# Kernel optimization log

Measured on AMD Instinct MI355X. Metric: run time of the kernel, lower is better.

The kernel has to match this reference:

```python
import math
import jax, jax.numpy as jnp
import numpy as np

K_EACH = 64
EPS = 1e-5
EPS_VAR = 1e-4
_GELU_C = math.sqrt(2.0 / math.pi)


def _gelu(x):
    return 0.5 * x * (1.0 + jnp.tanh(_GELU_C * (x + 0.044715 * x * x * x)))


def _topk_mask(score, k):
    # score: [B,T,D] -> bool mask [B,T,D] with True at the top-k per row
    B, T, D = score.shape
    idx = jax.lax.top_k(score, k)[1].reshape(B * T, k)
    rows = jnp.arange(B * T)[:, None]
    m = jnp.zeros((B * T, D), dtype=bool).at[rows, idx].set(True)
    return m.reshape(B, T, D)


def setup_inputs() -> dict:
    key = jax.random.key(0)
    ks = jax.random.split(key, 6)
    B, T, D = 4, 4096, 2048
    x = jax.random.normal(ks[0], (B, T, D), dtype=jnp.float32)
    ema_mean = 0.1 * jax.random.normal(ks[1], (D,), dtype=jnp.float32)
    ema_sq = ema_mean ** 2 + jax.random.uniform(ks[2], (D,), dtype=jnp.float32, minval=0.5, maxval=1.5)
    ema_out_mean = 0.1 * jax.random.normal(ks[3], (D,), dtype=jnp.float32)
    ema_out_sq = ema_out_mean ** 2 + jax.random.uniform(ks[4], (D,), dtype=jnp.float32, minval=0.5, maxval=1.5)
    d_raw = jax.random.normal(ks[5], (D,), dtype=jnp.float32)
    ema_out_dir = d_raw / jnp.linalg.norm(d_raw)
    return {
        "x": x,
        "logit_decay": jnp.asarray(math.log(0.9 / 0.1), jnp.float32),
        "log_tau": jnp.asarray(math.log(2.0), jnp.float32),
        "log_beta": jnp.asarray(math.log(math.exp(0.5) - 1.0), jnp.float32),
        "log_gamma": jnp.asarray(math.log(math.exp(1.0) - 1.0), jnp.float32),
        "ema_mean": ema_mean,
        "ema_sq": ema_sq,
        "ema_out_mean": ema_out_mean,
        "ema_out_sq": ema_out_sq,
        "ema_out_dir": ema_out_dir,
    }


def reference(x, logit_decay, log_tau, log_beta, log_gamma,
              ema_mean, ema_sq, ema_out_mean, ema_out_sq, ema_out_dir):
    # Steady-state (_ready=True) forward of GELU205. logit_decay only affects
    # the EMA state update (a no-grad side effect), not the returned output.
    sg = jax.lax.stop_gradient
    D = x.shape[-1]
    k = min(K_EACH, D)

    tau = jnp.exp(log_tau)
    beta = jax.nn.softplus(log_beta)
    gamma = jax.nn.softplus(log_gamma)

    out = _gelu(x)

    # per-channel z-scores against running stats (no-grad in original)
    var_in = jnp.maximum(ema_sq - ema_mean ** 2, EPS_VAR)
    z_in = sg((sg(x) - ema_mean) / (jnp.sqrt(var_in) + EPS))
    var_out = jnp.maximum(ema_out_sq - ema_out_mean ** 2, EPS_VAR)
    z_out = sg((sg(out) - ema_out_mean) / (jnp.sqrt(var_out) + EPS))

    # dual top-k intersection mask
    mask_in = _topk_mask(jnp.abs(z_in), k)
    mask_out = _topk_mask(jnp.abs(z_out), k)
    inter = mask_in & mask_out

    # channel gate (grads flow to beta, gamma; z_in is detached)
    inter_g = jnp.clip(1.0 + beta * jnp.tanh(gamma * z_in), 0.1, 8.0)
    gate_vec = jnp.where(inter, inter_g, 1.0)

    # cosine-similarity gate (fully no-grad in original, incl. tau)
    out_n = out / jnp.maximum(jnp.linalg.norm(out, axis=-1, keepdims=True), 1e-12)
    ema_n = ema_out_dir / jnp.maximum(jnp.linalg.norm(ema_out_dir), 1e-12)
    cos_sim = jnp.clip(jnp.sum(out_n * ema_n, axis=-1), -1.0, 1.0)
    gate_cos = sg(jnp.exp(-tau * cos_sim))[..., None]

    return out * gate_vec * gate_cos
```

## Files before the change

### kernel.cpp

```cpp
#include <hip/hip_runtime.h>
#include <math.h>
#include <stdint.h>

#define D_    2048
#define BLK   256
#define KSEL  64
#define NBIN  512
#define B0    96
#define CAP   128

typedef float v2f __attribute__((ext_vector_type(2)));

__device__ __forceinline__ float tanh_xla(float x) {
    const float kMax = 7.90531110763549805f;
    float xc = fminf(fmaxf(x, -kMax), kMax);
    float x2 = __fmul_rn(xc, xc);
    float p = -2.76076847742355e-16f;
    p = __fadd_rn(__fmul_rn(p, x2), 2.00018790482477e-13f);
    p = __fadd_rn(__fmul_rn(p, x2), -8.60467152213735e-11f);
    p = __fadd_rn(__fmul_rn(p, x2), 5.12229709037114e-08f);
    p = __fadd_rn(__fmul_rn(p, x2), 1.48572235717979e-05f);
    p = __fadd_rn(__fmul_rn(p, x2), 6.37261928875436e-04f);
    p = __fadd_rn(__fmul_rn(p, x2), 4.89352455891786e-03f);
    float num = __fmul_rn(xc, p);
    float q = 1.19825839466702e-06f;
    q = __fadd_rn(__fmul_rn(q, x2), 1.18534705686654e-04f);
    q = __fadd_rn(__fmul_rn(q, x2), 2.26843463243900e-03f);
    q = __fadd_rn(__fmul_rn(q, x2), 4.89352518554385e-03f);
    float r = __fdiv_rn(num, q);
    return (fabsf(x) < 0.0004f) ? x : r;
}

__device__ __forceinline__ float gelu_exact(float xx) {
    float a = __fmul_rn(0.044715f, xx);
    a = __fmul_rn(a, xx);
    a = __fmul_rn(a, xx);
    float inner = __fadd_rn(xx, a);
    float tg = tanh_xla(__fmul_rn(0.7978845608028654f, inner));
    return __fmul_rn(__fmul_rn(0.5f, xx), __fadd_rn(1.0f, tg));
}

__device__ __forceinline__ float tanh_fast(float y) {
    float e = __builtin_amdgcn_exp2f(y * 2.8853900817779268f);
    return 1.0f - 2.0f * __builtin_amdgcn_rcpf(1.0f + e);
}

__global__ __launch_bounds__(BLK) void prep_kernel(
    const float* __restrict__ m_in, const float* __restrict__ q_in,
    const float* __restrict__ m_out, const float* __restrict__ q_out,
    const float* __restrict__ dirv,
    const float* __restrict__ p_log_tau,
    const float* __restrict__ p_log_beta,
    const float* __restrict__ p_log_gamma,
    float* __restrict__ wsp)
{
    __shared__ float spart[4];
    const int t = threadIdx.x;
    const int c = blockIdx.x * BLK + t;
    if (c < D_) {
        float mi = m_in[c];
        float vi = fmaxf(__fsub_rn(q_in[c], __fmul_rn(mi, mi)), 1e-4f);
        float di = __fadd_rn(__fsqrt_rn(vi), 1e-5f);
        wsp[c]        = di;
        wsp[D_ + c]   = __fdiv_rn(1.0f, di);
        float mo = m_out[c];
        float vo = fmaxf(__fsub_rn(q_out[c], __fmul_rn(mo, mo)), 1e-4f);
        float dd = __fadd_rn(__fsqrt_rn(vo), 1e-5f);
        wsp[2 * D_ + c] = dd;
        wsp[3 * D_ + c] = __fdiv_rn(1.0f, dd);
    }
    if (blockIdx.x == 0) {
        float acc = 0.f;
        #pragma unroll
        for (int k = 0; k < D_ / BLK; ++k) {
            float v = dirv[t + k * BLK];
            acc = fmaf(v, v, acc);
        }
        #pragma unroll
        for (int off = 32; off > 0; off >>= 1) acc += __shfl_xor(acc, off);
        if ((t & 63) == 0) spart[t >> 6] = acc;
        __syncthreads();
        if (t == 0) {
            wsp[4 * D_ + 0] = spart[0] + spart[1] + spart[2] + spart[3];
            wsp[4 * D_ + 1] = expf(p_log_tau[0]);
            wsp[4 * D_ + 2] = log1pf(expf(p_log_beta[0]));
            wsp[4 * D_ + 3] = log1pf(expf(p_log_gamma[0]));
        }
    }
}

__device__ __forceinline__ void scan_find(
    const uint32_t* hist, int wid, int lane,
    int* sBi, int* sGi, int* sBo, int* sGo)
{
    if (wid < 2) {
        const uint32_t* hp = hist + wid * NBIN;
        uint32_t h[8];
        *(uint4*)&h[0] = *(const uint4*)&hp[lane * 8 + 0];
        *(uint4*)&h[4] = *(const uint4*)&hp[lane * 8 + 4];
        uint32_t tot = 0;
        #pragma unroll
        for (int k = 0; k < 8; ++k) tot += h[k];
        uint32_t S = tot;
        #pragma unroll
        for (int d2 = 1; d2 < 64; d2 <<= 1) {
            uint32_t o = __shfl_down(S, d2, 64);
            S += (lane + d2 < 64) ? o : 0u;
        }
        uint32_t run = S - tot;
        #pragma unroll
        for (int k = 7; k >= 0; --k) {
            uint32_t prev = run;
            run += h[k];
            if (run >= (uint32_t)KSEL && prev < (uint32_t)KSEL) {
                if (wid == 0) { *sBi = lane * 8 + k; *sGi = (int)prev; }
                else          { *sBo = lane * 8 + k; *sGo = (int)prev; }
            }
        }
    }
}

__global__ __launch_bounds__(BLK) void gelu205_kernel(
    const float* __restrict__ x,
    const float* __restrict__ ema_mean,
    const float* __restrict__ ema_out_mean,
    const float* __restrict__ ema_out_dir,
    const float* __restrict__ wsp,
    float* __restrict__ out)
{
    __shared__ uint32_t hist[2 * NBIN];
    __shared__ uint32_t cbI[CAP], ciI[CAP], cfI[CAP];
    __shared__ uint32_t cbO[CAP], ciO[CAP], cfO[CAP];
    __shared__ float sred[8];
    __shared__ float sgcos;
    __shared__ int sBi, sGi, sNCi, sBo, sGo, sNCo;

    const int t = threadIdx.x;
    const int row = blockIdx.x;
    const float* xr = x + (size_t)row * D_;
    float* outr = out + (size_t)row * D_;

    const float* den_in  = wsp;
    const float* inv_in  = wsp + D_;
    const float* den_out = wsp + 2 * D_;
    const float* inv_out = wsp + 3 * D_;
    const float dd_row = wsp[4 * D_ + 0];
    const float tau    = wsp[4 * D_ + 1];
    const float beta   = wsp[4 * D_ + 2];
    const float gamma  = wsp[4 * D_ + 3];

    float ov[8], zif[8];
    int bin_in[8], bin_out[8];
    v2f acc_oo = {0.f, 0.f}, acc_od = {0.f, 0.f};

    #pragma unroll
    for (int g = 0; g < 2; ++g) {
        const int base = (g << 10) + t * 4;
        float4 x4  = *(const float4*)(xr + base);
        float4 m4  = *(const float4*)(ema_mean + base);
        float4 i4  = *(const float4*)(inv_in + base);
        float4 mo4 = *(const float4*)(ema_out_mean + base);
        float4 io4 = *(const float4*)(inv_out + base);
        float4 d4  = *(const float4*)(ema_out_dir + base);
        const v2f* xp2  = (const v2f*)&x4;
        const v2f* mp2  = (const v2f*)&m4;
        const v2f* ip2  = (const v2f*)&i4;
        const v2f* mop2 = (const v2f*)&mo4;
        const v2f* iop2 = (const v2f*)&io4;
        const v2f* dp2  = (const v2f*)&d4;
        #pragma unroll
        for (int p = 0; p < 2; ++p) {
            const int j = g * 4 + p * 2;
            v2f xx = xp2[p];
            v2f x2 = xx * xx;
            v2f ax = xx * 0.044715f;
            v2f inner = __builtin_elementwise_fma(ax, x2, xx);
            v2f ea = inner * -2.3022269136469443f;
            v2f ev; ev.x = __builtin_amdgcn_exp2f(ea.x);
            ev.y = __builtin_amdgcn_exp2f(ea.y);
            v2f dn = ev + 1.0f;
            v2f sgm; sgm.x = __builtin_amdgcn_rcpf(dn.x);
            sgm.y = __builtin_amdgcn_rcpf(dn.y);
            v2f o2 = xx * sgm;
            ov[j] = o2.x; ov[j + 1] = o2.y;
            v2f zi2 = (xx - mp2[p]) * ip2[p];
            zif[j] = zi2.x; zif[j + 1] = zi2.y;
            bin_in[j]     = (int)fminf(fabsf(zi2.x) * 64.0f, 511.0f);
            bin_in[j + 1] = (int)fminf(fabsf(zi2.y) * 64.0f, 511.0f);
            v2f zo2 = (o2 - mop2[p]) * iop2[p];
            bin_out[j]     = (int)fminf(fabsf(zo2.x) * 64.0f, 511.0f);
            bin_out[j + 1] = (int)fminf(fabsf(zo2.y) * 64.0f, 511.0f);
            acc_oo = __builtin_elementwise_fma(o2, o2, acc_oo);
            acc_od = __builtin_elementwise_fma(o2, dp2[p], acc_od);
        }
    }
    float s_oo = acc_oo.x + acc_oo.y;
    float s_od = acc_od.x + acc_od.y;

    #pragma unroll
    for (int off = 32; off > 0; off >>= 1) {
        s_oo += __shfl_xor(s_oo, off);
        s_od += __shfl_xor(s_od, off);
    }
    const int wid = t >> 6, lane = t & 63;
    if (lane == 0) {
        sred[wid * 2 + 0] = s_oo;
        sred[wid * 2 + 1] = s_od;
    }

    *(uint4*)&hist[t * 4] = make_uint4(0u, 0u, 0u, 0u);
    if (t == 0) { sNCi = 0; sNCo = 0; sBi = -1; sBo = -1; }
    __syncthreads();

    #pragma unroll
    for (int j = 0; j < 8; ++j) {
        if (bin_in[j] >= B0)  atomicAdd(&hist[bin_in[j]], 1u);
        if (bin_out[j] >= B0) atomicAdd(&hist[NBIN + bin_out[j]], 1u);
    }
    if (t == 0) {
        float oo = sred[0] + sred[2] + sred[4] + sred[6];
        float od = sred[1] + sred[3] + sred[5] + sred[7];
        float no = fmaxf(sqrtf(oo), 1e-12f);
        float nd = fmaxf(sqrtf(dd_row), 1e-12f);
        float cs = fminf(fmaxf(od / (no * nd), -1.0f), 1.0f);
        sgcos = expf(-tau * cs);
    }
    __syncthreads();

    scan_find(hist, wid, lane, &sBi, &sGi, &sBo, &sGo);
    __syncthreads();

    int Bi = sBi, Bo = sBo;
    if (Bi < 0 || Bo < 0) {
        #pragma unroll
        for (int j = 0; j < 8; ++j) {
            if (bin_in[j] < B0)  atomicAdd(&hist[bin_in[j]], 1u);
            if (bin_out[j] < B0) atomicAdd(&hist[NBIN + bin_out[j]], 1u);
        }
        __syncthreads();
        scan_find(hist, wid, lane, &sBi, &sGi, &sBo, &sGo);
        __syncthreads();
        Bi = sBi; Bo = sBo;
    }

    int slotI[8], slotO[8];
    #pragma unroll
    for (int j = 0; j < 8; ++j) {
        slotI[j] = -1;
        slotO[j] = -1;
        const int ch = ((j >> 2) << 10) + t * 4 + (j & 3);
        if (bin_in[j] == Bi) {
            float xx = xr[ch];
            float ze = fabsf(__fdiv_rn(__fsub_rn(xx, ema_mean[ch]), den_in[ch]));
            int sl = atomicAdd(&sNCi, 1);
            if (sl < CAP) {
                cbI[sl] = __float_as_uint(ze);
                ciI[sl] = (uint32_t)ch;
                slotI[j] = sl;
            }
        }
        if (bin_out[j] == Bo) {
            float xx = xr[ch];
            float oe = gelu_exact(xx);
            float ze = fabsf(__fdiv_rn(__fsub_rn(oe, ema_out_mean[ch]), den_out[ch]));
            int sl = atomicAdd(&sNCo, 1);
            if (sl < CAP) {
                cbO[sl] = __float_as_uint(ze);
                ciO[sl] = (uint32_t)ch;
                slotO[j] = sl;
            }
        }
    }
    __syncthreads();

    {
        const int nci = min(sNCi, CAP), nco = min(sNCo, CAP);
        const uint32_t needI = (uint32_t)(KSEL - sGi);
        const uint32_t needO = (uint32_t)(KSEL - sGo);
        if (t < 128) {
            for (int i = t; i < nci; i += 128) {
                uint32_t ui = cbI[i], di = ciI[i], r = 0;
                for (int jj = 0; jj < nci; ++jj) {
                    uint32_t uj = cbI[jj];
                    r += (uj > ui || (uj == ui && ciI[jj] < di)) ? 1u : 0u;
                }
                cfI[i] = (r < needI) ? 1u : 0u;
            }
        } else {
            for (int i = t - 128; i < nco; i += 128) {
                uint32_t ui = cbO[i], di = ciO[i], r = 0;
                for (int jj = 0; jj < nco; ++jj) {
                    uint32_t uj = cbO[jj];
                    r += (uj > ui || (uj == ui && ciO[jj] < di)) ? 1u : 0u;
                }
                cfO[i] = (r < needO) ? 1u : 0u;
            }
        }
    }
    __syncthreads();

    const float gcos = sgcos;
    #pragma unroll
    for (int g = 0; g < 2; ++g) {
        float4 r4;
        float* rp = (float*)&r4;
        #pragma unroll
        for (int l = 0; l < 4; ++l) {
            const int j = g * 4 + l;
            bool selI = (bin_in[j] > Bi) || (slotI[j] >= 0 && cfI[slotI[j]] != 0u);
            bool selO = (bin_out[j] > Bo) || (slotO[j] >= 0 && cfO[slotO[j]] != 0u);
            float gate = 1.0f;
            if (selI && selO) {
                float th = tanh_fast(gamma * zif[j]);
                gate = fminf(fmaxf(fmaf(beta, th, 1.0f), 0.1f), 8.0f);
            }
            rp[l] = ov[j] * gate * gcos;
        }
        *(float4*)(outr + (g << 10) + t * 4) = r4;
    }
}

extern "C" void kernel_launch(void* const* d_in, const int* in_sizes, int n_in,
                              void* d_out, int out_size, void* d_ws, size_t ws_size,
                              hipStream_t stream) {
    const float* x            = (const float*)d_in[0];
    const float* p_log_tau    = (const float*)d_in[2];
    const float* p_log_beta   = (const float*)d_in[3];
    const float* p_log_gamma  = (const float*)d_in[4];
    const float* ema_mean     = (const float*)d_in[5];
    const float* ema_sq       = (const float*)d_in[6];
    const float* ema_out_mean = (const float*)d_in[7];
    const float* ema_out_sq   = (const float*)d_in[8];
    const float* ema_out_dir  = (const float*)d_in[9];
    float* wsp = (float*)d_ws;
    const int rows = in_sizes[0] / D_;

    prep_kernel<<<(D_ + BLK - 1) / BLK, BLK, 0, stream>>>(
        ema_mean, ema_sq, ema_out_mean, ema_out_sq, ema_out_dir,
        p_log_tau, p_log_beta, p_log_gamma, wsp);
    gelu205_kernel<<<rows, BLK, 0, stream>>>(
        x, ema_mean, ema_out_mean, ema_out_dir, wsp,
        (float*)d_out);
}
```

Baseline: 75.03 us.

## Process two rows per block with packed bins and per-wave scans

Each block now handles two rows, which halves the grid and shares the per-channel stat loads between the rows. Each of the four wavefronts scans one of the four histograms. The in and out bin indices are packed into one register, and per-element zif and slot arrays are replaced by a linear search of candidate channel lists plus recomputing z_in from global memory. The aim is to amortize setup and sync overhead and lower register pressure, at the cost of halving the block count to 8192 and adding a per-element candidate search.

New measurement: 122.4 us. 1.63x slower.

```diff
diff --git a/kernel.cpp b/kernel.cpp
--- a/kernel.cpp
+++ b/kernel.cpp
@@ -43,6 +43,32 @@
 __device__ __forceinline__ float tanh_fast(float y) {
     float e = __builtin_amdgcn_exp2f(y * 2.8853900817779268f);
     return 1.0f - 2.0f * __builtin_amdgcn_rcpf(1.0f + e);
+}
+
+__device__ __forceinline__ void elem2(
+    v2f xx, v2f m, v2f iv, v2f mo, v2f io, v2f dv,
+    float* ovp, uint32_t* bpp, v2f* aoo, v2f* aod)
+{
+    v2f x2 = xx * xx;
+    v2f ax = xx * 0.044715f;
+    v2f inner = __builtin_elementwise_fma(ax, x2, xx);
+    v2f ea = inner * -2.3022269136469443f;
+    v2f ev; ev.x = __builtin_amdgcn_exp2f(ea.x);
+    ev.y = __builtin_amdgcn_exp2f(ea.y);
+    v2f dn = ev + 1.0f;
+    v2f sg; sg.x = __builtin_amdgcn_rcpf(dn.x);
+    sg.y = __builtin_amdgcn_rcpf(dn.y);
+    v2f o2 = xx * sg;
+    ovp[0] = o2.x; ovp[1] = o2.y;
+    v2f zi = (xx - m) * iv;
+    v2f zo = (o2 - mo) * io;
+    v2f c511 = {511.0f, 511.0f};
+    v2f bi = __builtin_elementwise_min(__builtin_elementwise_abs(zi) * 64.0f, c511);
+    v2f bo = __builtin_elementwise_min(__builtin_elementwise_abs(zo) * 64.0f, c511);
+    bpp[0] = (uint32_t)(int)bi.x | ((uint32_t)(int)bo.x << 16);
+    bpp[1] = (uint32_t)(int)bi.y | ((uint32_t)(int)bo.y << 16);
+    *aoo = __builtin_elementwise_fma(o2, o2, *aoo);
+    *aod = __builtin_elementwise_fma(o2, dv, *aod);
 }
 
 __global__ __launch_bounds__(BLK) void prep_kernel(
@@ -89,35 +115,42 @@
     }
 }
 
-__device__ __forceinline__ void scan_find(
-    const uint32_t* hist, int wid, int lane,
-    int* sBi, int* sGi, int* sBo, int* sGo)
+__device__ __forceinline__ void scan_one(
+    const uint32_t* hp, volatile uint32_t* scr2, int lane)
 {
-    if (wid < 2) {
-        const uint32_t* hp = hist + wid * NBIN;
-        uint32_t h[8];
-        *(uint4*)&h[0] = *(const uint4*)&hp[lane * 8 + 0];
-        *(uint4*)&h[4] = *(const uint4*)&hp[lane * 8 + 4];
-        uint32_t tot = 0;
-        #pragma unroll
-        for (int k = 0; k < 8; ++k) tot += h[k];
-        uint32_t S = tot;
-        #pragma unroll
-        for (int d2 = 1; d2 < 64; d2 <<= 1) {
-            uint32_t o = __shfl_down(S, d2, 64);
-            S += (lane + d2 < 64) ? o : 0u;
-        }
-        uint32_t run = S - tot;
-        #pragma unroll
-        for (int k = 7; k >= 0; --k) {
-            uint32_t prev = run;
-            run += h[k];
-            if (run >= (uint32_t)KSEL && prev < (uint32_t)KSEL) {
-                if (wid == 0) { *sBi = lane * 8 + k; *sGi = (int)prev; }
-                else          { *sBo = lane * 8 + k; *sGo = (int)prev; }
-            }
-        }
-    }
+    uint32_t h[8];
+    *(uint4*)&h[0] = *(const uint4*)&hp[lane * 8 + 0];
+    *(uint4*)&h[4] = *(const uint4*)&hp[lane * 8 + 4];
+    uint32_t tot = 0;
+    #pragma unroll
+    for (int k = 0; k < 8; ++k) tot += h[k];
+    uint32_t S = tot;
+    #pragma unroll
+    for (int d = 1; d < 64; d <<= 1) {
+        uint32_t o = __shfl_down(S, d, 64);
+        S += (lane + d < 64) ? o : 0u;
+    }
+    uint32_t run = S - tot;
+    #pragma unroll
+    for (int k = 7; k >= 0; --k) {
+        uint32_t prev = run;
+        run += h[k];
+        if (run >= (uint32_t)KSEL && prev < (uint32_t)KSEL) {
+            scr2[0] = (uint32_t)(lane * 8 + k);
+            scr2[1] = prev;
+        }
+    }
+}
+
+__device__ __forceinline__ bool sel_one(
+    uint32_t bin, int B, const uint32_t* ci, const uint32_t* cf,
+    int nc, uint32_t ch)
+{
+    if ((int)bin > B) return true;
+    if ((int)bin != B) return false;
+    for (int jj = 0; jj < nc; ++jj)
+        if (ci[jj] == ch) return cf[jj] != 0u;
+    return false;
 }
 
 __global__ __launch_bounds__(BLK) void gelu205_kernel(
@@ -126,19 +159,22 @@
     const float* __restrict__ ema_out_mean,
     const float* __restrict__ ema_out_dir,
     const float* __restrict__ wsp,
-    float* __restrict__ out)
+    float* __restrict__ out,
+    int nrows)
 {
-    __shared__ uint32_t hist[2 * NBIN];
-    __shared__ uint32_t cbI[CAP], ciI[CAP], cfI[CAP];
-    __shared__ uint32_t cbO[CAP], ciO[CAP], cfO[CAP];
-    __shared__ float sred[8];
-    __shared__ float sgcos;
-    __shared__ int sBi, sGi, sNCi, sBo, sGo, sNCo;
+    __shared__ uint32_t lds[2048 + 4 * 3 * CAP + 16];
+    uint32_t* hist = lds;
+    uint32_t* scr  = lds + 2048 + 4 * 3 * CAP;
 
     const int t = threadIdx.x;
-    const int row = blockIdx.x;
-    const float* xr = x + (size_t)row * D_;
-    float* outr = out + (size_t)row * D_;
+    const int lane = t & 63, wid = t >> 6;
+    const int r0 = blockIdx.x * 2, r1 = r0 + 1;
+    const bool has2 = (r1 < nrows);
+
+    const float* xr0 = x + (size_t)r0 * D_;
+    const float* xr1 = x + (size_t)r1 * D_;
+    float* outr0 = out + (size_t)r0 * D_;
+    float* outr1 = out + (size_t)r1 * D_;
 
     const float* den_in  = wsp;
     const float* inv_in  = wsp + D_;
@@ -149,174 +185,228 @@
     const float beta   = wsp[4 * D_ + 2];
     const float gamma  = wsp[4 * D_ + 3];
 
-    float ov[8], zif[8];
-    int bin_in[8], bin_out[8];
-    v2f acc_oo = {0.f, 0.f}, acc_od = {0.f, 0.f};
+    {
+        uint4 z4 = make_uint4(0u, 0u, 0u, 0u);
+        *(uint4*)&hist[t * 8 + 0] = z4;
+        *(uint4*)&hist[t * 8 + 4] = z4;
+    }
+    if (t < 12) scr[t] = (t < 8 && (t & 1) == 0) ? 0xffffffffu : 0u;
+
+    float ov0[8], ov1[8];
+    uint32_t bp0[8], bp1[8];
+    v2f aoo0 = {0.f, 0.f}, aod0 = {0.f, 0.f};
+    v2f aoo1 = {0.f, 0.f}, aod1 = {0.f, 0.f};
 
     #pragma unroll
     for (int g = 0; g < 2; ++g) {
-        const int base = (g << 10) + t * 4;
-        float4 x4  = *(const float4*)(xr + base);
+        const int base = (g << 10) + (t << 2);
         float4 m4  = *(const float4*)(ema_mean + base);
         float4 i4  = *(const float4*)(inv_in + base);
         float4 mo4 = *(const float4*)(ema_out_mean + base);
         float4 io4 = *(const float4*)(inv_out + base);
         float4 d4  = *(const float4*)(ema_out_dir + base);
-        const v2f* xp2  = (const v2f*)&x4;
+        float4 xa  = *(const float4*)(xr0 + base);
+        float4 xb;
+        if (has2) xb = *(const float4*)(xr1 + base);
+        else xb = make_float4(0.f, 0.f, 0.f, 0.f);
         const v2f* mp2  = (const v2f*)&m4;
         const v2f* ip2  = (const v2f*)&i4;
         const v2f* mop2 = (const v2f*)&mo4;
         const v2f* iop2 = (const v2f*)&io4;
         const v2f* dp2  = (const v2f*)&d4;
+        const v2f* xa2  = (const v2f*)&xa;
+        const v2f* xb2  = (const v2f*)&xb;
         #pragma unroll
         for (int p = 0; p < 2; ++p) {
             const int j = g * 4 + p * 2;
-            v2f xx = xp2[p];
-            v2f x2 = xx * xx;
-            v2f ax = xx * 0.044715f;
-            v2f inner = __builtin_elementwise_fma(ax, x2, xx);
-            v2f ea = inner * -2.3022269136469443f;
-            v2f ev; ev.x = __builtin_amdgcn_exp2f(ea.x);
-            ev.y = __builtin_amdgcn_exp2f(ea.y);
-            v2f dn = ev + 1.0f;
-            v2f sgm; sgm.x = __builtin_amdgcn_rcpf(dn.x);
-            sgm.y = __builtin_amdgcn_rcpf(dn.y);
-            v2f o2 = xx * sgm;
-            ov[j] = o2.x; ov[j + 1] = o2.y;
-            v2f zi2 = (xx - mp2[p]) * ip2[p];
-            zif[j] = zi2.x; zif[j + 1] = zi2.y;
-            bin_in[j]     = (int)fminf(fabsf(zi2.x) * 64.0f, 511.0f);
-            bin_in[j + 1] = (int)fminf(fabsf(zi2.y) * 64.0f, 511.0f);
-            v2f zo2 = (o2 - mop2[p]) * iop2[p];
-            bin_out[j]     = (int)fminf(fabsf(zo2.x) * 64.0f, 511.0f);
-            bin_out[j + 1] = (int)fminf(fabsf(zo2.y) * 64.0f, 511.0f);
-            acc_oo = __builtin_elementwise_fma(o2, o2, acc_oo);
-            acc_od = __builtin_elementwise_fma(o2, dp2[p], acc_od);
-        }
-    }
-    float s_oo = acc_oo.x + acc_oo.y;
-    float s_od = acc_od.x + acc_od.y;
-
+            elem2(xa2[p], mp2[p], ip2[p], mop2[p], iop2[p], dp2[p],
+                  &ov0[j], &bp0[j], &aoo0, &aod0);
+            elem2(xb2[p], mp2[p], ip2[p], mop2[p], iop2[p], dp2[p],
+                  &ov1[j], &bp1[j], &aoo1, &aod1);
+        }
+    }
+
+    float oo0 = aoo0.x + aoo0.y, od0 = aod0.x + aod0.y;
+    float oo1 = aoo1.x + aoo1.y, od1 = aod1.x + aod1.y;
     #pragma unroll
     for (int off = 32; off > 0; off >>= 1) {
-        s_oo += __shfl_xor(s_oo, off);
-        s_od += __shfl_xor(s_od, off);
-    }
-    const int wid = t >> 6, lane = t & 63;
+        oo0 += __shfl_xor(oo0, off);
+        od0 += __shfl_xor(od0, off);
+        oo1 += __shfl_xor(oo1, off);
+        od1 += __shfl_xor(od1, off);
+    }
+    __shared__ float sred[16];
     if (lane == 0) {
-        sred[wid * 2 + 0] = s_oo;
-        sred[wid * 2 + 1] = s_od;
-    }
-
-    *(uint4*)&hist[t * 4] = make_uint4(0u, 0u, 0u, 0u);
-    if (t == 0) { sNCi = 0; sNCo = 0; sBi = -1; sBo = -1; }
+        sred[wid * 4 + 0] = oo0;
+        sred[wid * 4 + 1] = od0;
+        sred[wid * 4 + 2] = oo1;
+        sred[wid * 4 + 3] = od1;
+    }
     __syncthreads();
 
+    float gcos0, gcos1;
+    {
+        float foo0 = sred[0] + sred[4] + sred[8] + sred[12];
+        float fod0 = sred[1] + sred[5] + sred[9] + sred[13];
+        float foo1 = sred[2] + sred[6] + sred[10] + sred[14];
+        float fod1 = sred[3] + sred[7] + sred[11] + sred[15];
+        float nd = fmaxf(sqrtf(dd_row), 1e-12f);
+        float no0 = fmaxf(sqrtf(foo0), 1e-12f);
+        float cs0 = fminf(fmaxf(fod0 / (no0 * nd), -1.0f), 1.0f);
+        gcos0 = expf(-tau * cs0);
+        float no1 = fmaxf(sqrtf(foo1), 1e-12f);
+        float cs1 = fminf(fmaxf(fod1 / (no1 * nd), -1.0f), 1.0f);
+        gcos1 = expf(-tau * cs1);
+    }
+
     #pragma unroll
     for (int j = 0; j < 8; ++j) {
-        if (bin_in[j] >= B0)  atomicAdd(&hist[bin_in[j]], 1u);
-        if (bin_out[j] >= B0) atomicAdd(&hist[NBIN + bin_out[j]], 1u);
-    }
-    if (t == 0) {
-        float oo = sred[0] + sred[2] + sred[4] + sred[6];
-        float od = sred[1] + sred[3] + sred[5] + sred[7];
-        float no = fmaxf(sqrtf(oo), 1e-12f);
-        float nd = fmaxf(sqrtf(dd_row), 1e-12f);
-        float cs = fminf(fmaxf(od / (no * nd), -1.0f), 1.0f);
-        sgcos = expf(-tau * cs);
+        uint32_t bi = bp0[j] & 0xffffu, bo = bp0[j] >> 16;
+        if (bi >= (uint32_t)B0) atomicAdd(&hist[bi], 1u);
+        if (bo >= (uint32_t)B0) atomicAdd(&hist[NBIN + bo], 1u);
+    }
+    if (has2) {
+        #pragma unroll
+        for (int j = 0; j < 8; ++j) {
+            uint32_t bi = bp1[j] & 0xffffu, bo = bp1[j] >> 16;
+            if (bi >= (uint32_t)B0) atomicAdd(&hist[2 * NBIN + bi], 1u);
+            if (bo >= (uint32_t)B0) atomicAdd(&hist[3 * NBIN + bo], 1u);
+        }
     }
     __syncthreads();
 
-    scan_find(hist, wid, lane, &sBi, &sGi, &sBo, &sGo);
+    scan_one(hist + wid * NBIN, scr + 2 * wid, lane);
     __syncthreads();
 
-    int Bi = sBi, Bo = sBo;
-    if (Bi < 0 || Bo < 0) {
+    int BI0 = (int)scr[0], BO0 = (int)scr[2];
+    int BI1 = (int)scr[4], BO1 = (int)scr[6];
+
+    bool fb = (BI0 < 0) | (BO0 < 0) | (has2 & ((BI1 < 0) | (BO1 < 0)));
+    if (fb) {
         #pragma unroll
         for (int j = 0; j < 8; ++j) {
-            if (bin_in[j] < B0)  atomicAdd(&hist[bin_in[j]], 1u);
-            if (bin_out[j] < B0) atomicAdd(&hist[NBIN + bin_out[j]], 1u);
+            uint32_t bi = bp0[j] & 0xffffu, bo = bp0[j] >> 16;
+            if (BI0 < 0 && bi < (uint32_t)B0) atomicAdd(&hist[bi], 1u);
+            if (BO0 < 0 && bo < (uint32_t)B0) atomicAdd(&hist[NBIN + bo], 1u);
+        }
+        if (has2) {
+            #pragma unroll
+            for (int j = 0; j < 8; ++j) {
+                uint32_t bi = bp1[j] & 0xffffu, bo = bp1[j] >> 16;
+                if (BI1 < 0 && bi < (uint32_t)B0) atomicAdd(&hist[2 * NBIN + bi], 1u);
+                if (BO1 < 0 && bo < (uint32_t)B0) atomicAdd(&hist[3 * NBIN + bo], 1u);
+            }
         }
         __syncthreads();
-        scan_find(hist, wid, lane, &sBi, &sGi, &sBo, &sGo);
+        scan_one(hist + wid * NBIN, scr + 2 * wid, lane);
         __syncthreads();
-        Bi = sBi; Bo = sBo;
-    }
-
-    int slotI[8], slotO[8];
+        BI0 = (int)scr[0]; BO0 = (int)scr[2];
+        BI1 = (int)scr[4]; BO1 = (int)scr[6];
+    }
+
+    uint32_t* cb0 = lds + 2048;
+    uint32_t* cb1 = cb0 + 3 * CAP;
+    uint32_t* cb2 = cb1 + 3 * CAP;
+    uint32_t* cb3 = cb2 + 3 * CAP;
+
     #pragma unroll
     for (int j = 0; j < 8; ++j) {
-        slotI[j] = -1;
-        slotO[j] = -1;
-        const int ch = ((j >> 2) << 10) + t * 4 + (j & 3);
-        if (bin_in[j] == Bi) {
-            float xx = xr[ch];
+        const int ch = ((j >> 2) << 10) + (t << 2) + (j & 3);
+        if ((int)(bp0[j] & 0xffffu) == BI0) {
+            float xx = xr0[ch];
             float ze = fabsf(__fdiv_rn(__fsub_rn(xx, ema_mean[ch]), den_in[ch]));
-            int sl = atomicAdd(&sNCi, 1);
-            if (sl < CAP) {
-                cbI[sl] = __float_as_uint(ze);
-                ciI[sl] = (uint32_t)ch;
-                slotI[j] = sl;
-            }
-        }
-        if (bin_out[j] == Bo) {
-            float xx = xr[ch];
+            uint32_t sl = atomicAdd(&scr[8], 1u);
+            if (sl < CAP) { cb0[sl] = __float_as_uint(ze); cb0[CAP + sl] = (uint32_t)ch; }
+        }
+        if ((int)(bp0[j] >> 16) == BO0) {
+            float xx = xr0[ch];
             float oe = gelu_exact(xx);
             float ze = fabsf(__fdiv_rn(__fsub_rn(oe, ema_out_mean[ch]), den_out[ch]));
-            int sl = atomicAdd(&sNCo, 1);
-            if (sl < CAP) {
-                cbO[sl] = __float_as_uint(ze);
-                ciO[sl] = (uint32_t)ch;
-                slotO[j] = sl;
+            uint32_t sl = atomicAdd(&scr[9], 1u);
+            if (sl < CAP) { cb1[sl] = __float_as_uint(ze); cb1[CAP + sl] = (uint32_t)ch; }
+        }
+        if (has2) {
+            if ((int)(bp1[j] & 0xffffu) == BI1) {
+                float xx = xr1[ch];
+                float ze = fabsf(__fdiv_rn(__fsub_rn(xx, ema_mean[ch]), den_in[ch]));
+                uint32_t sl = atomicAdd(&scr[10], 1u);
+                if (sl < CAP) { cb2[sl] = __float_as_uint(ze); cb2[CAP + sl] = (uint32_t)ch; }
+            }
+            if ((int)(bp1[j] >> 16) == BO1) {
+                float xx = xr1[ch];
+                float oe = gelu_exact(xx);
+                float ze = fabsf(__fdiv_rn(__fsub_rn(oe, ema_out_mean[ch]), den_out[ch]));
+                uint32_t sl = atomicAdd(&scr[11], 1u);
+                if (sl < CAP) { cb3[sl] = __float_as_uint(ze); cb3[CAP + sl] = (uint32_t)ch; }
             }
         }
     }
     __syncthreads();
 
     {
-        const int nci = min(sNCi, CAP), nco = min(sNCo, CAP);
-        const uint32_t needI = (uint32_t)(KSEL - sGi);
-        const uint32_t needO = (uint32_t)(KSEL - sGo);
-        if (t < 128) {
-            for (int i = t; i < nci; i += 128) {
-                uint32_t ui = cbI[i], di = ciI[i], r = 0;
-                for (int jj = 0; jj < nci; ++jj) {
-                    uint32_t uj = cbI[jj];
-                    r += (uj > ui || (uj == ui && ciI[jj] < di)) ? 1u : 0u;
+        uint32_t* cbw = lds + 2048 + wid * 3 * CAP;
+        int Bw = (int)scr[2 * wid];
+        if (Bw >= 0) {
+            const int nc = min((int)scr[8 + wid], CAP);
+            const uint32_t need = (uint32_t)(KSEL - (int)scr[2 * wid + 1]);
+            for (int i = lane; i < nc; i += 64) {
+                uint32_t ui = cbw[i], di = cbw[CAP + i], r = 0;
+                for (int jj = 0; jj < nc; ++jj) {
+                    uint32_t uj = cbw[jj];
+                    r += (uj > ui || (uj == ui && cbw[CAP + jj] < di)) ? 1u : 0u;
                 }
-                cfI[i] = (r < needI) ? 1u : 0u;
-            }
-        } else {
-            for (int i = t - 128; i < nco; i += 128) {
-                uint32_t ui = cbO[i], di = ciO[i], r = 0;
-                for (int jj = 0; jj < nco; ++jj) {
-                    uint32_t uj = cbO[jj];
-                    r += (uj > ui || (uj == ui && ciO[jj] < di)) ? 1u : 0u;
-                }
-                cfO[i] = (r < needO) ? 1u : 0u;
+                cbw[2 * CAP + i] = (r < need) ? 1u : 0u;
             }
         }
     }
     __syncthreads();
 
-    const float gcos = sgcos;
-    #pragma unroll
-    for (int g = 0; g < 2; ++g) {
+    const int nc0 = min((int)scr[8], CAP),  nc1 = min((int)scr[9], CAP);
+    const int nc2 = min((int)scr[10], CAP), nc3 = min((int)scr[11], CAP);
+
+    #pragma unroll
+    for (int k = 0; k < 2; ++k) {
         float4 r4;
         float* rp = (float*)&r4;
         #pragma unroll
         for (int l = 0; l < 4; ++l) {
-            const int j = g * 4 + l;
-            bool selI = (bin_in[j] > Bi) || (slotI[j] >= 0 && cfI[slotI[j]] != 0u);
-            bool selO = (bin_out[j] > Bo) || (slotO[j] >= 0 && cfO[slotO[j]] != 0u);
+            const int j = k * 4 + l;
+            const uint32_t ch = (uint32_t)(((j >> 2) << 10) + (t << 2) + (j & 3));
+            bool selI = sel_one(bp0[j] & 0xffffu, BI0, cb0 + CAP, cb0 + 2 * CAP, nc0, ch);
+            bool selO = sel_one(bp0[j] >> 16,     BO0, cb1 + CAP, cb1 + 2 * CAP, nc1, ch);
             float gate = 1.0f;
             if (selI && selO) {
-                float th = tanh_fast(gamma * zif[j]);
+                float xx = xr0[ch];
+                float zi = (xx - ema_mean[ch]) * inv_in[ch];
+                float th = tanh_fast(gamma * zi);
                 gate = fminf(fmaxf(fmaf(beta, th, 1.0f), 0.1f), 8.0f);
             }
-            rp[l] = ov[j] * gate * gcos;
-        }
-        *(float4*)(outr + (g << 10) + t * 4) = r4;
+            rp[l] = ov0[j] * gate * gcos0;
+        }
+        *(float4*)(outr0 + (k << 10) + (t << 2)) = r4;
+    }
+    if (has2) {
+        #pragma unroll
+        for (int k = 0; k < 2; ++k) {
+            float4 r4;
+            float* rp = (float*)&r4;
+            #pragma unroll
+            for (int l = 0; l < 4; ++l) {
+                const int j = k * 4 + l;
+                const uint32_t ch = (uint32_t)(((j >> 2) << 10) + (t << 2) + (j & 3));
+                bool selI = sel_one(bp1[j] & 0xffffu, BI1, cb2 + CAP, cb2 + 2 * CAP, nc2, ch);
+                bool selO = sel_one(bp1[j] >> 16,     BO1, cb3 + CAP, cb3 + 2 * CAP, nc3, ch);
+                float gate = 1.0f;
+                if (selI && selO) {
+                    float xx = xr1[ch];
+                    float zi = (xx - ema_mean[ch]) * inv_in[ch];
+                    float th = tanh_fast(gamma * zi);
+                    gate = fminf(fmaxf(fmaf(beta, th, 1.0f), 0.1f), 8.0f);
+                }
+                rp[l] = ov1[j] * gate * gcos1;
+            }
+            *(float4*)(outr1 + (k << 10) + (t << 2)) = r4;
+        }
     }
 }
 
@@ -338,7 +428,7 @@
     prep_kernel<<<(D_ + BLK - 1) / BLK, BLK, 0, stream>>>(
         ema_mean, ema_sq, ema_out_mean, ema_out_sq, ema_out_dir,
         p_log_tau, p_log_beta, p_log_gamma, wsp);
-    gelu205_kernel<<<rows, BLK, 0, stream>>>(
+    gelu205_kernel<<<(rows + 1) / 2, BLK, 0, stream>>>(
         x, ema_mean, ema_out_mean, ema_out_dir, wsp,
-        (float*)d_out);
-}
+        (float*)d_out, rows);
+}
```

## Process multiple rows per block with prefetch of next row's input

Applied to the files above, without the earlier changes.

Each block now handles 8 rows in a loop instead of one, and prefetches the next row's x values into registers while the current row's histogram and selection phases run. This aims to hide global load latency behind the synchronization-heavy top-k phases and to amortize block launch overhead. In exchange the grid shrinks from 16384 to 2048 blocks, which could reduce latency hiding from concurrent blocks and leave tail imbalance across CUs.

After: 176.1 us. +134.7%, slower.

```diff
diff --git a/kernel.cpp b/kernel.cpp
--- a/kernel.cpp
+++ b/kernel.cpp
@@ -8,6 +8,7 @@
 #define NBIN  512
 #define B0    96
 #define CAP   128
+#define RPB   8
 
 typedef float v2f __attribute__((ext_vector_type(2)));
 
@@ -126,7 +127,8 @@
     const float* __restrict__ ema_out_mean,
     const float* __restrict__ ema_out_dir,
     const float* __restrict__ wsp,
-    float* __restrict__ out)
+    float* __restrict__ out,
+    int nrows)
 {
     __shared__ uint32_t hist[2 * NBIN];
     __shared__ uint32_t cbI[CAP], ciI[CAP], cfI[CAP];
@@ -136,187 +138,207 @@
     __shared__ int sBi, sGi, sNCi, sBo, sGo, sNCo;
 
     const int t = threadIdx.x;
-    const int row = blockIdx.x;
-    const float* xr = x + (size_t)row * D_;
-    float* outr = out + (size_t)row * D_;
-
-    const float* den_in  = wsp;
-    const float* inv_in  = wsp + D_;
-    const float* den_out = wsp + 2 * D_;
-    const float* inv_out = wsp + 3 * D_;
-    const float dd_row = wsp[4 * D_ + 0];
-    const float tau    = wsp[4 * D_ + 1];
-    const float beta   = wsp[4 * D_ + 2];
-    const float gamma  = wsp[4 * D_ + 3];
-
-    float ov[8], zif[8];
-    int bin_in[8], bin_out[8];
-    v2f acc_oo = {0.f, 0.f}, acc_od = {0.f, 0.f};
-
-    #pragma unroll
-    for (int g = 0; g < 2; ++g) {
-        const int base = (g << 10) + t * 4;
-        float4 x4  = *(const float4*)(xr + base);
-        float4 m4  = *(const float4*)(ema_mean + base);
-        float4 i4  = *(const float4*)(inv_in + base);
-        float4 mo4 = *(const float4*)(ema_out_mean + base);
-        float4 io4 = *(const float4*)(inv_out + base);
-        float4 d4  = *(const float4*)(ema_out_dir + base);
-        const v2f* xp2  = (const v2f*)&x4;
-        const v2f* mp2  = (const v2f*)&m4;
-        const v2f* ip2  = (const v2f*)&i4;
-        const v2f* mop2 = (const v2f*)&mo4;
-        const v2f* iop2 = (const v2f*)&io4;
-        const v2f* dp2  = (const v2f*)&d4;
-        #pragma unroll
-        for (int p = 0; p < 2; ++p) {
-            const int j = g * 4 + p * 2;
-            v2f xx = xp2[p];
-            v2f x2 = xx * xx;
-            v2f ax = xx * 0.044715f;
-            v2f inner = __builtin_elementwise_fma(ax, x2, xx);
-            v2f ea = inner * -2.3022269136469443f;
-            v2f ev; ev.x = __builtin_amdgcn_exp2f(ea.x);
-            ev.y = __builtin_amdgcn_exp2f(ea.y);
-            v2f dn = ev + 1.0f;
-            v2f sgm; sgm.x = __builtin_amdgcn_rcpf(dn.x);
-            sgm.y = __builtin_amdgcn_rcpf(dn.y);
-            v2f o2 = xx * sgm;
-            ov[j] = o2.x; ov[j + 1] = o2.y;
-            v2f zi2 = (xx - mp2[p]) * ip2[p];
-            zif[j] = zi2.x; zif[j + 1] = zi2.y;
-            bin_in[j]     = (int)fminf(fabsf(zi2.x) * 64.0f, 511.0f);
-            bin_in[j + 1] = (int)fminf(fabsf(zi2.y) * 64.0f, 511.0f);
-            v2f zo2 = (o2 - mop2[p]) * iop2[p];
-            bin_out[j]     = (int)fminf(fabsf(zo2.x) * 64.0f, 511.0f);
-            bin_out[j + 1] = (int)fminf(fabsf(zo2.y) * 64.0f, 511.0f);
-            acc_oo = __builtin_elementwise_fma(o2, o2, acc_oo);
-            acc_od = __builtin_elementwise_fma(o2, dp2[p], acc_od);
-        }
-    }
-    float s_oo = acc_oo.x + acc_oo.y;
-    float s_od = acc_od.x + acc_od.y;
-
-    #pragma unroll
-    for (int off = 32; off > 0; off >>= 1) {
-        s_oo += __shfl_xor(s_oo, off);
-        s_od += __shfl_xor(s_od, off);
-    }
-    const int wid = t >> 6, lane = t & 63;
-    if (lane == 0) {
-        sred[wid * 2 + 0] = s_oo;
-        sred[wid * 2 + 1] = s_od;
-    }
-
-    *(uint4*)&hist[t * 4] = make_uint4(0u, 0u, 0u, 0u);
-    if (t == 0) { sNCi = 0; sNCo = 0; sBi = -1; sBo = -1; }
-    __syncthreads();
-
-    #pragma unroll
-    for (int j = 0; j < 8; ++j) {
-        if (bin_in[j] >= B0)  atomicAdd(&hist[bin_in[j]], 1u);
-        if (bin_out[j] >= B0) atomicAdd(&hist[NBIN + bin_out[j]], 1u);
-    }
-    if (t == 0) {
-        float oo = sred[0] + sred[2] + sred[4] + sred[6];
-        float od = sred[1] + sred[3] + sred[5] + sred[7];
-        float no = fmaxf(sqrtf(oo), 1e-12f);
-        float nd = fmaxf(sqrtf(dd_row), 1e-12f);
-        float cs = fminf(fmaxf(od / (no * nd), -1.0f), 1.0f);
-        sgcos = expf(-tau * cs);
-    }
-    __syncthreads();
-
-    scan_find(hist, wid, lane, &sBi, &sGi, &sBo, &sGo);
-    __syncthreads();
-
-    int Bi = sBi, Bo = sBo;
-    if (Bi < 0 || Bo < 0) {
+    const int lane = t & 63, wid = t >> 6;
+    const int row0 = blockIdx.x * RPB;
+    if (row0 >= nrows) return;
+
+    float4 xn0, xn1;
+    {
+        const float* xr = x + (size_t)row0 * D_;
+        xn0 = *(const float4*)(xr + (t << 2));
+        xn1 = *(const float4*)(xr + 1024 + (t << 2));
+    }
+
+    for (int k = 0; k < RPB; ++k) {
+        const int row = row0 + k;
+        if (row >= nrows) break;
+        const float* xr = x + (size_t)row * D_;
+        float* outr = out + (size_t)row * D_;
+
+        asm volatile("" ::: "memory");
+
+        const float dd_row = wsp[4 * D_ + 0];
+        const float tau    = wsp[4 * D_ + 1];
+        const float beta   = wsp[4 * D_ + 2];
+        const float gamma  = wsp[4 * D_ + 3];
+
+        float4 xcur[2];
+        xcur[0] = xn0;
+        xcur[1] = xn1;
+
+        float ov[8], zif[8];
+        int bin_in[8], bin_out[8];
+        v2f acc_oo = {0.f, 0.f}, acc_od = {0.f, 0.f};
+
+        #pragma unroll
+        for (int g = 0; g < 2; ++g) {
+            const int base = (g << 10) + (t << 2);
+            float4 m4  = *(const float4*)(ema_mean + base);
+            float4 i4  = *(const float4*)(wsp + D_ + base);
+            float4 mo4 = *(const float4*)(ema_out_mean + base);
+            float4 io4 = *(const float4*)(wsp + 3 * D_ + base);
+            float4 d4  = *(const float4*)(ema_out_dir + base);
+            const v2f* xp2  = (const v2f*)&xcur[g];
+            const v2f* mp2  = (const v2f*)&m4;
+            const v2f* ip2  = (const v2f*)&i4;
+            const v2f* mop2 = (const v2f*)&mo4;
+            const v2f* iop2 = (const v2f*)&io4;
+            const v2f* dp2  = (const v2f*)&d4;
+            #pragma unroll
+            for (int p = 0; p < 2; ++p) {
+                const int j = g * 4 + p * 2;
+                v2f xx = xp2[p];
+                v2f x2 = xx * xx;
+                v2f ax = xx * 0.044715f;
+                v2f inner = __builtin_elementwise_fma(ax, x2, xx);
+                v2f ea = inner * -2.3022269136469443f;
+                v2f ev; ev.x = __builtin_amdgcn_exp2f(ea.x);
+                ev.y = __builtin_amdgcn_exp2f(ea.y);
+                v2f dn = ev + 1.0f;
+                v2f sgm; sgm.x = __builtin_amdgcn_rcpf(dn.x);
+                sgm.y = __builtin_amdgcn_rcpf(dn.y);
+                v2f o2 = xx * sgm;
+                ov[j] = o2.x; ov[j + 1] = o2.y;
+                v2f zi2 = (xx - mp2[p]) * ip2[p];
+                zif[j] = zi2.x; zif[j + 1] = zi2.y;
+                bin_in[j]     = (int)fminf(fabsf(zi2.x) * 64.0f, 511.0f);
+                bin_in[j + 1] = (int)fminf(fabsf(zi2.y) * 64.0f, 511.0f);
+                v2f zo2 = (o2 - mop2[p]) * iop2[p];
+                bin_out[j]     = (int)fminf(fabsf(zo2.x) * 64.0f, 511.0f);
+                bin_out[j + 1] = (int)fminf(fabsf(zo2.y) * 64.0f, 511.0f);
+                acc_oo = __builtin_elementwise_fma(o2, o2, acc_oo);
+                acc_od = __builtin_elementwise_fma(o2, dp2[p], acc_od);
+            }
+        }
+
+        if (k + 1 < RPB && row + 1 < nrows) {
+            const float* xrn = x + (size_t)(row + 1) * D_;
+            xn0 = *(const float4*)(xrn + (t << 2));
+            xn1 = *(const float4*)(xrn + 1024 + (t << 2));
+        }
+
+        float s_oo = acc_oo.x + acc_oo.y;
+        float s_od = acc_od.x + acc_od.y;
+        #pragma unroll
+        for (int off = 32; off > 0; off >>= 1) {
+            s_oo += __shfl_xor(s_oo, off);
+            s_od += __shfl_xor(s_od, off);
+        }
+        if (lane == 0) {
+            sred[wid * 2 + 0] = s_oo;
+            sred[wid * 2 + 1] = s_od;
+        }
+
+        *(uint4*)&hist[t * 4] = make_uint4(0u, 0u, 0u, 0u);
+        if (t == 0) { sNCi = 0; sNCo = 0; sBi = -1; sBo = -1; }
+        __syncthreads();
+
         #pragma unroll
         for (int j = 0; j < 8; ++j) {
-            if (bin_in[j] < B0)  atomicAdd(&hist[bin_in[j]], 1u);
-            if (bin_out[j] < B0) atomicAdd(&hist[NBIN + bin_out[j]], 1u);
-        }
-        __syncthreads();
+            if (bin_in[j] >= B0)  atomicAdd(&hist[bin_in[j]], 1u);
+            if (bin_out[j] >= B0) atomicAdd(&hist[NBIN + bin_out[j]], 1u);
+        }
+        if (t == 0) {
+            float oo = sred[0] + sred[2] + sred[4] + sred[6];
+            float od = sred[1] + sred[3] + sred[5] + sred[7];
+            float no = fmaxf(sqrtf(oo), 1e-12f);
+            float nd = fmaxf(sqrtf(dd_row), 1e-12f);
+            float cs = fminf(fmaxf(od / (no * nd), -1.0f), 1.0f);
+            sgcos = expf(-tau * cs);
+        }
+        __syncthreads();
+
         scan_find(hist, wid, lane, &sBi, &sGi, &sBo, &sGo);
         __syncthreads();
-        Bi = sBi; Bo = sBo;
-    }
-
-    int slotI[8], slotO[8];
-    #pragma unroll
-    for (int j = 0; j < 8; ++j) {
-        slotI[j] = -1;
-        slotO[j] = -1;
-        const int ch = ((j >> 2) << 10) + t * 4 + (j & 3);
-        if (bin_in[j] == Bi) {
-            float xx = xr[ch];
-            float ze = fabsf(__fdiv_rn(__fsub_rn(xx, ema_mean[ch]), den_in[ch]));
-            int sl = atomicAdd(&sNCi, 1);
-            if (sl < CAP) {
-                cbI[sl] = __float_as_uint(ze);
-                ciI[sl] = (uint32_t)ch;
-                slotI[j] = sl;
-            }
-        }
-        if (bin_out[j] == Bo) {
-            float xx = xr[ch];
-            float oe = gelu_exact(xx);
-            float ze = fabsf(__fdiv_rn(__fsub_rn(oe, ema_out_mean[ch]), den_out[ch]));
-            int sl = atomicAdd(&sNCo, 1);
-            if (sl < CAP) {
-                cbO[sl] = __float_as_uint(ze);
-                ciO[sl] = (uint32_t)ch;
-                slotO[j] = sl;
-            }
-        }
-    }
-    __syncthreads();
-
-    {
-        const int nci = min(sNCi, CAP), nco = min(sNCo, CAP);
-        const uint32_t needI = (uint32_t)(KSEL - sGi);
-        const uint32_t needO = (uint32_t)(KSEL - sGo);
-        if (t < 128) {
-            for (int i = t; i < nci; i += 128) {
-                uint32_t ui = cbI[i], di = ciI[i], r = 0;
-                for (int jj = 0; jj < nci; ++jj) {
-                    uint32_t uj = cbI[jj];
-                    r += (uj > ui || (uj == ui && ciI[jj] < di)) ? 1u : 0u;
-                }
-                cfI[i] = (r < needI) ? 1u : 0u;
-            }
-        } else {
-            for (int i = t - 128; i < nco; i += 128) {
-                uint32_t ui = cbO[i], di = ciO[i], r = 0;
-                for (int jj = 0; jj < nco; ++jj) {
-                    uint32_t uj = cbO[jj];
-                    r += (uj > ui || (uj == ui && ciO[jj] < di)) ? 1u : 0u;
-                }
-                cfO[i] = (r < needO) ? 1u : 0u;
-            }
-        }
-    }
-    __syncthreads();
-
-    const float gcos = sgcos;
-    #pragma unroll
-    for (int g = 0; g < 2; ++g) {
-        float4 r4;
-        float* rp = (float*)&r4;
-        #pragma unroll
-        for (int l = 0; l < 4; ++l) {
-            const int j = g * 4 + l;
-            bool selI = (bin_in[j] > Bi) || (slotI[j] >= 0 && cfI[slotI[j]] != 0u);
-            bool selO = (bin_out[j] > Bo) || (slotO[j] >= 0 && cfO[slotO[j]] != 0u);
-            float gate = 1.0f;
-            if (selI && selO) {
-                float th = tanh_fast(gamma * zif[j]);
-                gate = fminf(fmaxf(fmaf(beta, th, 1.0f), 0.1f), 8.0f);
-            }
-            rp[l] = ov[j] * gate * gcos;
-        }
-        *(float4*)(outr + (g << 10) + t * 4) = r4;
+
+        int Bi = sBi, Bo = sBo;
+        if (Bi < 0 || Bo < 0) {
+            #pragma unroll
+            for (int j = 0; j < 8; ++j) {
+                if (bin_in[j] < B0)  atomicAdd(&hist[bin_in[j]], 1u);
+                if (bin_out[j] < B0) atomicAdd(&hist[NBIN + bin_out[j]], 1u);
+            }
+            __syncthreads();
+            scan_find(hist, wid, lane, &sBi, &sGi, &sBo, &sGo);
+            __syncthreads();
+            Bi = sBi; Bo = sBo;
+        }
+
+        int slotI[8], slotO[8];
+        #pragma unroll
+        for (int j = 0; j < 8; ++j) {
+            slotI[j] = -1;
+            slotO[j] = -1;
+            const int ch = ((j >> 2) << 10) + (t << 2) + (j & 3);
+            if (bin_in[j] == Bi) {
+                float xx = xr[ch];
+                float ze = fabsf(__fdiv_rn(__fsub_rn(xx, ema_mean[ch]), wsp[ch]));
+                int sl = atomicAdd(&sNCi, 1);
+                if (sl < CAP) {
+                    cbI[sl] = __float_as_uint(ze);
+                    ciI[sl] = (uint32_t)ch;
+                    slotI[j] = sl;
+                }
+            }
+            if (bin_out[j] == Bo) {
+                float xx = xr[ch];
+                float oe = gelu_exact(xx);
+                float ze = fabsf(__fdiv_rn(__fsub_rn(oe, ema_out_mean[ch]), wsp[2 * D_ + ch]));
+                int sl = atomicAdd(&sNCo, 1);
+                if (sl < CAP) {
+                    cbO[sl] = __float_as_uint(ze);
+                    ciO[sl] = (uint32_t)ch;
+                    slotO[j] = sl;
+                }
+            }
+        }
+        __syncthreads();
+
+        {
+            const int nci = min(sNCi, CAP), nco = min(sNCo, CAP);
+            const uint32_t needI = (uint32_t)(KSEL - sGi);
+            const uint32_t needO = (uint32_t)(KSEL - sGo);
+            if (t < 128) {
+                for (int i = t; i < nci; i += 128) {
+                    uint32_t ui = cbI[i], di = ciI[i], r = 0;
+                    for (int jj = 0; jj < nci; ++jj) {
+                        uint32_t uj = cbI[jj];
+                        r += (uj > ui || (uj == ui && ciI[jj] < di)) ? 1u : 0u;
+                    }
+                    cfI[i] = (r < needI) ? 1u : 0u;
+                }
+            } else {
+                for (int i = t - 128; i < nco; i += 128) {
+                    uint32_t ui = cbO[i], di = ciO[i], r = 0;
+                    for (int jj = 0; jj < nco; ++jj) {
+                        uint32_t uj = cbO[jj];
+                        r += (uj > ui || (uj == ui && ciO[jj] < di)) ? 1u : 0u;
+                    }
+                    cfO[i] = (r < needO) ? 1u : 0u;
+                }
+            }
+        }
+        __syncthreads();
+
+        const float gcos = sgcos;
+        #pragma unroll
+        for (int g = 0; g < 2; ++g) {
+            float4 r4;
+            float* rp = (float*)&r4;
+            #pragma unroll
+            for (int l = 0; l < 4; ++l) {
+                const int j = g * 4 + l;
+                bool selI = (bin_in[j] > Bi) || (slotI[j] >= 0 && cfI[slotI[j]] != 0u);
+                bool selO = (bin_out[j] > Bo) || (slotO[j] >= 0 && cfO[slotO[j]] != 0u);
+                float gate = 1.0f;
+                if (selI && selO) {
+                    float th = tanh_fast(gamma * zif[j]);
+                    gate = fminf(fmaxf(fmaf(beta, th, 1.0f), 0.1f), 8.0f);
+                }
+                rp[l] = ov[j] * gate * gcos;
+            }
+            *(float4*)(outr + (g << 10) + (t << 2)) = r4;
+        }
     }
 }
 
@@ -338,7 +360,7 @@
     prep_kernel<<<(D_ + BLK - 1) / BLK, BLK, 0, stream>>>(
         ema_mean, ema_sq, ema_out_mean, ema_out_sq, ema_out_dir,
         p_log_tau, p_log_beta, p_log_gamma, wsp);
-    gelu205_kernel<<<rows, BLK, 0, stream>>>(
+    gelu205_kernel<<<(rows + RPB - 1) / RPB, BLK, 0, stream>>>(
         x, ema_mean, ema_out_mean, ema_out_dir, wsp,
-        (float*)d_out);
-}
+        (float*)d_out, rows);
+}
```
